# Optimization experiments

Measured on AMD Instinct MI355X. Metric: run time of the kernel, lower is better.

## Reference

```python
import jax, jax.numpy as jnp
import numpy as np
import math

R = 3  # search_radius
GROUPS = 4

def _conv(x, w):
    return jax.lax.conv_general_dilated(x, w, (1, 1), 'SAME',
                                        dimension_numbers=('NCHW', 'OIHW', 'NCHW'))

def _gn(x, g, b, eps=1e-5):
    B, C, H, W = x.shape
    xr = x.reshape(B, GROUPS, C // GROUPS, H, W)
    m = xr.mean(axis=(2, 3, 4), keepdims=True)
    v = xr.var(axis=(2, 3, 4), keepdims=True)
    xn = ((xr - m) * jax.lax.rsqrt(v + eps)).reshape(B, C, H, W)
    return xn * g.reshape(1, C, 1, 1) + b.reshape(1, C, 1, 1)

def _gelu(x):
    return jax.nn.gelu(x, approximate=False)

def _encode(x, W0, Ws, G, Bt):
    x = _gelu(_gn(_conv(x, W0), G[0], Bt[0]))
    for i in range(Ws.shape[0]):  # fixed depth-1 layers
        x = _gelu(_gn(_conv(x, Ws[i]), G[i + 1], Bt[i + 1]))
    return x

def _center_w(h, w):
    y = jnp.linspace(-1.0, 1.0, h)
    x = jnp.linspace(-1.0, 1.0, w)
    yy, xx = jnp.meshgrid(y, x, indexing='ij')
    g = jnp.exp(-(yy ** 2 + xx ** 2) / (2 * 0.5 ** 2))
    return (g / g.sum())[None, None]  # [1,1,H,W]

def _l2n(x):  # F.normalize(dim=1, eps=1e-6)
    n = jnp.sqrt(jnp.sum(x * x, axis=1, keepdims=True))
    return x / jnp.maximum(n, 1e-6)

def setup_inputs() -> dict:
    key = jax.random.key(0)
    ks = jax.random.split(key, 24)
    B, Cr, H, W, Ch, MH = 256, 6, 64, 64, 32, 128
    depth = 4
    feat_dim = Ch * 3 + 2
    s = 0.05
    return {
        'rubin_patch': jax.random.normal(ks[0], (B, Cr, H, W), jnp.float32),
        'vis_patch': jax.random.normal(ks[1], (B, 1, H, W), jnp.float32),
        'pixel_to_sky': jax.random.normal(ks[2], (B, 2, 2), jnp.float32),
        'rW0': jax.random.normal(ks[3], (Ch, Cr, 3, 3), jnp.float32) * s,
        'rWs': jax.random.normal(ks[4], (depth - 1, Ch, Ch, 3, 3), jnp.float32) * s,
        'rG': 1.0 + jax.random.normal(ks[5], (depth, Ch), jnp.float32) * s,
        'rBt': jax.random.normal(ks[6], (depth, Ch), jnp.float32) * s,
        'vW0': jax.random.normal(ks[7], (Ch, 1, 3, 3), jnp.float32) * s,
        'vWs': jax.random.normal(ks[8], (depth - 1, Ch, Ch, 3, 3), jnp.float32) * s,
        'vG': 1.0 + jax.random.normal(ks[9], (depth, Ch), jnp.float32) * s,
        'vBt': jax.random.normal(ks[10], (depth, Ch), jnp.float32) * s,
        'projR': jax.random.normal(ks[11], (Ch, Ch), jnp.float32) * s,
        'projV': jax.random.normal(ks[12], (Ch, Ch), jnp.float32) * s,
        'log_temp': jnp.array(math.log(0.05), jnp.float32),
        'W1': jax.random.normal(ks[13], (feat_dim, MH), jnp.float32) * s,
        'b1': jax.random.normal(ks[14], (MH,), jnp.float32) * s,
        'W2': jax.random.normal(ks[15], (MH, MH), jnp.float32) * s,
        'b2': jax.random.normal(ks[16], (MH,), jnp.float32) * s,
        'W3': jax.random.normal(ks[17], (MH, 3), jnp.float32) * s,
        'b3': jax.random.normal(ks[18], (3,), jnp.float32) * s,
    }

def _forward(rubin_patch, vis_patch, pixel_to_sky, rW0, rWs, rG, rBt,
             vW0, vWs, vG, vBt, projR, projV, log_temp,
             W1, b1, W2, b2, W3, b3):
    rubin_feat = _encode(rubin_patch, rW0, rWs, rG, rBt)  # [B,C,H,W]
    vis_feat = _encode(vis_patch, vW0, vWs, vG, vBt)
    B, C, H, W = rubin_feat.shape

    # --- weighted cross-correlation cost volume ---
    rubin_n = _l2n(jnp.einsum('oc,bchw->bohw', projR, rubin_feat))
    vis_n = _l2n(jnp.einsum('oc,bchw->bohw', projV, vis_feat))
    rubin_energy = jnp.sum(rubin_n * rubin_n, axis=1, keepdims=True)
    gauss = _center_w(H, W)
    sw = rubin_energy * gauss
    sw = sw / (jnp.sum(sw, axis=(2, 3), keepdims=True) + 1e-8)
    rw = rubin_n * sw  # fold weights into rubin features once
    vis_pad = jnp.pad(vis_n, ((0, 0), (0, 0), (R, R), (R, R)), mode='edge')
    scale = 1.0 / math.sqrt(float(C))
    logits = []
    for dy in range(-R, R + 1):
        for dx in range(-R, R + 1):
            sh = vis_pad[:, :, R + dy:R + dy + H, R + dx:R + dx + W]
            logits.append(jnp.sum(rw * sh, axis=(1, 2, 3)) * scale)
    logits = jnp.stack(logits, axis=1)  # [B,(2R+1)^2]

    dx_lut = jnp.array([float(dx) for dy in range(-R, R + 1) for dx in range(-R, R + 1)], jnp.float32)
    dy_lut = jnp.array([float(dy) for dy in range(-R, R + 1) for dx in range(-R, R + 1)], jnp.float32)
    temp = jnp.maximum(jnp.exp(log_temp), 1e-3)
    probs = jax.nn.softmax(logits / temp, axis=1)
    coarse_dx = jnp.sum(probs * dx_lut[None], axis=1)
    coarse_dy = jnp.sum(probs * dy_lut[None], axis=1)

    # --- center-biased pooling + MLP refine ---
    rp = jnp.sum(rubin_feat * gauss, axis=(2, 3))  # [B,C]
    vp = jnp.sum(vis_feat * gauss, axis=(2, 3))
    pooled = jnp.concatenate([rp, vp, rp - vp,
                              jnp.stack([coarse_dx, coarse_dy], axis=1)], axis=1)
    h = _gelu(pooled @ W1 + b1)
    h = _gelu(h @ W2 + b2)
    res = h @ W3 + b3  # [B,3]

    dx_px = coarse_dx + res[:, 0]
    dy_px = coarse_dy + res[:, 1]
    log_sigma = jnp.clip(res[:, 2], -6.0, 3.0)
    pix = jnp.stack([dx_px, dy_px], axis=1)
    pred_sky = jnp.einsum('bij,bj->bi', pixel_to_sky, pix)
    # pack all differentiable outputs: [dx, dy, pred_sky(2), log_sigma, logits(49)]
    return jnp.concatenate([dx_px[:, None], dy_px[:, None], pred_sky,
                            log_sigma[:, None], logits], axis=1)  # [B,54]

def reference(rubin_patch, vis_patch, pixel_to_sky, rW0, rWs, rG, rBt,
              vW0, vWs, vG, vBt, projR, projV, log_temp,
              W1, b1, W2, b2, W3, b3):
    return _forward(rubin_patch, vis_patch, pixel_to_sky, rW0, rWs, rG, rBt,
                    vW0, vWs, vG, vBt, projR, projV, log_temp,
                    W1, b1, W2, b2, W3, b3)
```

## Files before the change

### kernel.cpp

```cpp
#include <hip/hip_runtime.h>
#include <math.h>

#define HW 4096
#define NB 256

typedef __attribute__((ext_vector_type(8))) short bf16x8_t;
typedef __attribute__((ext_vector_type(16))) float f32x16_t;

__device__ __forceinline__ float gelu_f(float x) {
    float z = x * 0.70710678118654752440f;
    float az = fabsf(z);
    float t = 1.0f / fmaf(0.3275911f, az, 1.0f);
    float p = t * fmaf(t, fmaf(t, fmaf(t, fmaf(t, 1.061405429f, -1.453152027f),
                                       1.421413741f), -0.284496736f), 0.254829592f);
    float e = __expf(-az * az);
    float er = 1.0f - p * e;
    er = copysignf(er, z);
    return 0.5f * x * (1.0f + er);
}
__device__ __forceinline__ unsigned short f2bf(float f) {
    unsigned int u = __float_as_uint(f);
    unsigned int r = u + 0x7FFFu + ((u >> 16) & 1u);
    return (unsigned short)(r >> 16);
}
__device__ __forceinline__ float bf2f(unsigned short h) {
    return __uint_as_float(((unsigned int)h) << 16);
}


__global__ __launch_bounds__(256) void gauss_kernel(float* __restrict__ gauss) {
    __shared__ float sg[HW];
    __shared__ float sR[4];
    int tid = threadIdx.x;
    float part = 0.0f;
    for (int p = tid; p < HW; p += 256) {
        int y = p >> 6, x = p & 63;
        float yy = -1.0f + (2.0f / 63.0f) * (float)y;
        float xx = -1.0f + (2.0f / 63.0f) * (float)x;
        float g = expf(-(yy * yy + xx * xx) * 2.0f);
        sg[p] = g;
        part += g;
    }
#pragma unroll
    for (int off = 32; off > 0; off >>= 1) part += __shfl_down(part, off);
    if ((tid & 63) == 0) sR[tid >> 6] = part;
    __syncthreads();
    float invt = 1.0f / (sR[0] + sR[1] + sR[2] + sR[3]);
    for (int p = tid; p < HW; p += 256) gauss[p] = sg[p] * invt;
}

__global__ __launch_bounds__(256) void prep_w_kernel(
    const float* __restrict__ rWs, const float* __restrict__ vWs,
    const float* __restrict__ rW0, const float* __restrict__ vW0,
    unsigned short* __restrict__ wq) {
    int i = blockIdx.x * 256 + threadIdx.x;
    if (i >= 115712) return;
    float wv;
    if (i < 110592) {
        int j = i & 7;
        int lane = (i >> 3) & 63;
        int f = i >> 9;
        int hl = f & 1, k2 = (f >> 1) & 1, tap = (f >> 2) % 9, layer = (f >> 2) / 9;
        int co = lane & 31, hf = lane >> 5;
        int ci = k2 * 16 + hf * 8 + j;
        int ky = tap / 3, kx = tap % 3;
        wv = (layer < 3)
            ? rWs[(((size_t)layer * 32 + co) * 32 + ci) * 9 + ky * 3 + kx]
            : vWs[(((size_t)(layer - 3) * 32 + co) * 32 + ci) * 9 + ky * 3 + kx];
        unsigned short h = f2bf(wv);
        unsigned short l = f2bf(wv - bf2f(h));
        wq[i] = hl ? l : h;
        return;
    }
    int i2 = i - 110592;
    int j = i2 & 7;
    int lane = (i2 >> 3) & 63;
    int co = lane & 31, hf = lane >> 5;
    if (i2 < 4096) {
        int f = i2 >> 9;
        int hl = f & 1, ks = f >> 1;
        int q = ks * 16 + hf * 8 + j;
        wv = (q < 54) ? rW0[((size_t)co * 6 + q / 9) * 9 + q % 9] : 0.0f;
        unsigned short h = f2bf(wv);
        unsigned short l = f2bf(wv - bf2f(h));
        wq[i] = hl ? l : h;
    } else {
        int i3 = i2 - 4096;
        int f = i3 >> 9;
        int q = hf * 8 + j;
        wv = (q < 9) ? vW0[(size_t)co * 9 + q] : 0.0f;
        unsigned short h = f2bf(wv);
        unsigned short l = f2bf(wv - bf2f(h));
        wq[i] = f ? l : h;
    }
}

template <int CIN>
__global__ __launch_bounds__(128) void conv_first_m_kernel(
    const float* __restrict__ in, const unsigned short* __restrict__ wq0,
    unsigned short* __restrict__ qout, float* __restrict__ statp) {
    constexpr int KQ = CIN * 9;
    constexpr int KS = (KQ + 15) / 16;
    const int b = blockIdx.y;
    const int strip = blockIdx.x;
    const int tid = threadIdx.x;
    const int wv = tid >> 6;
    const int lane = tid & 63;
    const int m = lane & 31;
    const int hf = lane >> 5;
    const int xh32 = wv * 32;

    __shared__ __align__(16) char smem[20736];
    __shared__ float sRed[2][8];
    float* sInF = (float*)smem;

    const int y0 = strip * 4;
    const float* inb = in + (size_t)b * CIN * HW;
    for (int idx = tid; idx < CIN * 6 * 66; idx += 128) {
        int ci = idx / 396;
        int rem = idx - ci * 396;
        int r = rem / 66;
        int col = rem - r * 66;
        int gy = y0 - 1 + r;
        int gx = col - 1;
        float v = 0.0f;
        if (gy >= 0 && gy < 64 && gx >= 0 && gx < 64) v = inb[ci * HW + gy * 64 + gx];
        sInF[ci * 396 + r * 66 + col] = v;
    }

    int P[KS][8];
#pragma unroll
    for (int ks = 0; ks < KS; ++ks)
#pragma unroll
        for (int j = 0; j < 8; ++j) {
            int q = ks * 16 + hf * 8 + j;
            int ci = q / 9, tap = q - ci * 9;
            int ky = tap / 3, kx = tap - ky * 3;
            P[ks][j] = (q < KQ) ? (ci * 396 + ky * 66 + kx) : 0;
        }
    bf16x8_t Wf[KS][2];
#pragma unroll
    for (int ks = 0; ks < KS; ++ks)
#pragma unroll
        for (int hl = 0; hl < 2; ++hl)
            Wf[ks][hl] = __builtin_bit_cast(
                bf16x8_t, *(const uint4*)(wq0 + (size_t)(ks * 2 + hl) * 512 + lane * 8));
    __syncthreads();

    f32x16_t acc[4];
#pragma unroll
    for (int i = 0; i < 4; ++i)
#pragma unroll
        for (int j = 0; j < 16; ++j) acc[i][j] = 0.0f;

    const int xcol = xh32 + m;
#pragma unroll
    for (int orow = 0; orow < 4; ++orow) {
        const int obase = orow * 66 + xcol;
#pragma unroll
        for (int ks = 0; ks < KS; ++ks) {
            unsigned int pk[4];
#pragma unroll
            for (int e = 0; e < 4; ++e) {
                float v0 = sInF[P[ks][e * 2] + obase];
                float v1 = sInF[P[ks][e * 2 + 1] + obase];
                pk[e] = (unsigned)f2bf(v0) | ((unsigned)f2bf(v1) << 16);
            }
            uint4 u; u.x = pk[0]; u.y = pk[1]; u.z = pk[2]; u.w = pk[3];
            bf16x8_t A = __builtin_bit_cast(bf16x8_t, u);
            acc[orow] = __builtin_amdgcn_mfma_f32_32x32x16_bf16(A, Wf[ks][0], acc[orow], 0, 0, 0);
            acc[orow] = __builtin_amdgcn_mfma_f32_32x32x16_bf16(A, Wf[ks][1], acc[orow], 0, 0, 0);
        }
    }

    __syncthreads();
    unsigned short* lds_t = (unsigned short*)smem;
    const int co = lane & 31;
    float s1 = 0.0f, s2 = 0.0f;
#pragma unroll
    for (int orow = 0; orow < 4; ++orow) {
#pragma unroll
        for (int r = 0; r < 16; ++r) {
            int mm = (r & 3) + 8 * (r >> 2) + 4 * hf;
            int pxl = (orow << 6) + xh32 + mm;
            float v = acc[orow][r];
            s1 += v;
            s2 = fmaf(v, v, s2);
            lds_t[pxl * 40 + co] = f2bf(v);
        }
    }
    s1 += __shfl_xor(s1, 32); s2 += __shfl_xor(s2, 32);
    s1 += __shfl_xor(s1, 1);  s2 += __shfl_xor(s2, 1);
    s1 += __shfl_xor(s1, 2);  s2 += __shfl_xor(s2, 2);
    s1 += __shfl_xor(s1, 4);  s2 += __shfl_xor(s2, 4);
    if (lane < 32 && (lane & 7) == 0) {
        sRed[wv][co >> 3] = s1;
        sRed[wv][4 + (co >> 3)] = s2;
    }
    __syncthreads();
    if (tid < 8) statp[((size_t)b * 16 + strip) * 8 + tid] = sRed[0][tid] + sRed[1][tid];

    char* qb = (char*)qout + (size_t)b * 4 * HW * 16;
    const int p0 = y0 * 64;
#pragma unroll
    for (int pi = 0; pi < 2; ++pi) {
        int p = pi * 128 + tid;
#pragma unroll
        for (int s = 0; s < 4; ++s) {
            uint4 uh = *(const uint4*)(lds_t + p * 40 + s * 8);
            *(uint4*)(qb + ((size_t)(s * HW) + p0 + p) * 16) = uh;
        }
    }
}

__global__ __launch_bounds__(256) void gn_finalize_kernel(
    const float* __restrict__ statp, const float* __restrict__ gma,
    const float* __restrict__ bta, float* __restrict__ coef, int n, int ns) {
    int i = blockIdx.x * 256 + threadIdx.x;
    if (i >= n) return;
    int b = i >> 5, c = i & 31, g = c >> 3;
    float s1 = 0.0f, s2 = 0.0f;
    for (int s = 0; s < ns; ++s) {
        s1 += statp[((size_t)b * 16 + s) * 8 + g];
        s2 += statp[((size_t)b * 16 + s) * 8 + 4 + g];
    }
    const float invN = 1.0f / 32768.0f;
    float mean = s1 * invN;
    float var = s2 * invN - mean * mean;
    float rstd = rsqrtf(var + 1e-5f);
    float a = rstd * gma[c];
    float bb = bta[c] - mean * a;
    coef[i * 2 + 0] = a;
    coef[i * 2 + 1] = bb;
}

#define SLOT 80
#define ROWB (66 * SLOT)
__global__ __launch_bounds__(256) void convm_kernel(
    const unsigned short* __restrict__ qin, const float* __restrict__ coef,
    const unsigned short* __restrict__ wq,
    unsigned short* __restrict__ qout, float* __restrict__ statp) {
    const int b = blockIdx.y;
    const int strip = blockIdx.x;
    const int tid = threadIdx.x;
    const int wv = tid >> 6;
    const int lane = tid & 63;
    const int m = lane & 31;
    const int hf = lane >> 5;

    __shared__ __align__(16) char sQ[10 * ROWB];
    __shared__ float sRed[4][8];
    __shared__ float sc[64];

    const int y0 = strip * 8;
    const char* img = (const char*)qin + (size_t)b * 4 * HW * 16;

    if (tid < 64) sc[tid] = coef[b * 64 + tid];
    if (tid < 80) {
        int r = tid >> 3, side = (tid >> 2) & 1, sub = tid & 3;
        uint4 z; z.x = z.y = z.z = z.w = 0;
        *(uint4*)(sQ + r * ROWB + side * 65 * SLOT + sub * 16) = z;
    }
    __syncthreads();

    const int px = tid & 63;
    const int s_id = tid >> 6;
    const int rot = px & 3;
    float ca[8], cb[8];
#pragma unroll
    for (int e = 0; e < 8; ++e) {
        ca[e] = sc[(s_id * 8 + e) * 2 + 0];
        cb[e] = sc[(s_id * 8 + e) * 2 + 1];
    }
    uint4 ld[10];
#pragma unroll
    for (int r = 0; r < 10; ++r) {
        int gy = y0 - 1 + r;
        if (gy >= 0 && gy < 64) {
            ld[r] = *(const uint4*)(img + ((size_t)(s_id * HW) + gy * 64 + px) * 16);
        } else {
            ld[r].x = ld[r].y = ld[r].z = ld[r].w = 0;
        }
    }
    char* dstc = sQ + (px + 1) * SLOT + ((s_id + rot) & 3) * 16;
#pragma unroll
    for (int r = 0; r < 10; ++r) {
        unsigned int hd[4] = {ld[r].x, ld[r].y, ld[r].z, ld[r].w};
        unsigned int ho[4];
#pragma unroll
        for (int e = 0; e < 4; ++e) {
            float x0 = bf2f((unsigned short)(hd[e] & 0xFFFF));
            float x1 = bf2f((unsigned short)(hd[e] >> 16));
            float y0v = gelu_f(fmaf(ca[e * 2], x0, cb[e * 2]));
            float y1v = gelu_f(fmaf(ca[e * 2 + 1], x1, cb[e * 2 + 1]));
            ho[e] = (unsigned)f2bf(y0v) | ((unsigned)f2bf(y1v) << 16);
        }
        uint4 oh; oh.x = ho[0]; oh.y = ho[1]; oh.z = ho[2]; oh.w = ho[3];
        *(uint4*)(dstc + r * ROWB) = oh;
    }
    __syncthreads();

    const int rq = wv & 1;
    const int xh32 = (wv >> 1) * 32;
    f32x16_t acc[4];
#pragma unroll
    for (int i = 0; i < 4; ++i)
#pragma unroll
        for (int j = 0; j < 16; ++j) acc[i][j] = 0.0f;

    for (int kx = 0; kx < 3; ++kx) {
        bf16x8_t Wf[3][2];
#pragma unroll
        for (int ky = 0; ky < 3; ++ky)
#pragma unroll
            for (int k2 = 0; k2 < 2; ++k2) {
                int fi = (((ky * 3 + kx) * 2 + k2) * 2);
                Wf[ky][k2] = __builtin_bit_cast(
                    bf16x8_t, *(const uint4*)(wq + (size_t)fi * 512 + lane * 8));
            }
        const int slotb = xh32 + kx + m;
        const int prot = (m + kx + 3) & 3;
#pragma unroll
        for (int li = 0; li < 6; ++li) {
            const char* rowp = sQ + (rq * 4 + li) * ROWB + slotb * SLOT;
            bf16x8_t Ah[2];
#pragma unroll
            for (int k2 = 0; k2 < 2; ++k2) {
                int s = k2 * 2 + hf;
                Ah[k2] = __builtin_bit_cast(bf16x8_t, *(const uint4*)(rowp + ((s + prot) & 3) * 16));
            }
#pragma unroll
            for (int ky = 0; ky < 3; ++ky) {
                int orow = li - ky;
                if (orow < 0 || orow > 3) continue;
#pragma unroll
                for (int k2 = 0; k2 < 2; ++k2)
                    acc[orow] = __builtin_amdgcn_mfma_f32_32x32x16_bf16(Ah[k2], Wf[ky][k2], acc[orow], 0, 0, 0);
            }
        }
    }

    __syncthreads();
    unsigned short* lds_t = (unsigned short*)sQ;
    const int co = lane & 31;
    float s1 = 0.0f, s2 = 0.0f;
#pragma unroll
    for (int orow = 0; orow < 4; ++orow) {
#pragma unroll
        for (int r = 0; r < 16; ++r) {
            int mm = (r & 3) + 8 * (r >> 2) + 4 * hf;
            int pxl = (rq * 4 + orow) * 64 + xh32 + mm;
            float v = acc[orow][r];
            s1 += v;
            s2 = fmaf(v, v, s2);
            lds_t[pxl * 40 + co] = f2bf(v);
        }
    }
    s1 += __shfl_xor(s1, 32); s2 += __shfl_xor(s2, 32);
    s1 += __shfl_xor(s1, 1);  s2 += __shfl_xor(s2, 1);
    s1 += __shfl_xor(s1, 2);  s2 += __shfl_xor(s2, 2);
    s1 += __shfl_xor(s1, 4);  s2 += __shfl_xor(s2, 4);
    if (lane < 32 && (lane & 7) == 0) {
        sRed[wv][co >> 3] = s1;
        sRed[wv][4 + (co >> 3)] = s2;
    }
    __syncthreads();
    if (tid < 8)
        statp[((size_t)b * 16 + strip) * 8 + tid] =
            sRed[0][tid] + sRed[1][tid] + sRed[2][tid] + sRed[3][tid];

    char* qb = (char*)qout + (size_t)b * 4 * HW * 16;
    const int p0 = y0 * 64;
#pragma unroll
    for (int pi = 0; pi < 2; ++pi) {
        int p = pi * 256 + tid;
#pragma unroll
        for (int s = 0; s < 4; ++s) {
            uint4 uh = *(const uint4*)(lds_t + p * 40 + s * 8);
            *(uint4*)(qb + ((size_t)(s * HW) + p0 + p) * 16) = uh;
        }
    }
}

__global__ __launch_bounds__(256) void proj_kernel(
    const unsigned short* __restrict__ q, const float* __restrict__ coef,
    const float* __restrict__ pw, unsigned short* __restrict__ outn,
    float* __restrict__ poolp, float* __restrict__ E, float* __restrict__ swp,
    const float* __restrict__ gauss, int vpad) {
    int b = blockIdx.y, chunk = blockIdx.x, tid = threadIdx.x;
    int p = chunk * 256 + tid;
    __shared__ float sR[4];
    __shared__ float sc[64];
    __shared__ float red[32][257];
    if (tid < 64) sc[tid] = coef[b * 64 + tid];
    __syncthreads();
    float feat[32];
    {
        const char* qb = (const char*)q + (size_t)b * 4 * HW * 16;
#pragma unroll
        for (int s = 0; s < 4; ++s) {
            uint4 uh = *(const uint4*)(qb + ((size_t)(s * HW) + p) * 16);
            unsigned int hd[4] = {uh.x, uh.y, uh.z, uh.w};
#pragma unroll
            for (int e = 0; e < 4; ++e) {
                int c0 = s * 8 + e * 2;
                float x0 = bf2f((unsigned short)(hd[e] & 0xFFFF));
                float x1 = bf2f((unsigned short)(hd[e] >> 16));
                feat[c0] = gelu_f(fmaf(sc[c0 * 2], x0, sc[c0 * 2 + 1]));
                feat[c0 + 1] = gelu_f(fmaf(sc[(c0 + 1) * 2], x1, sc[(c0 + 1) * 2 + 1]));
            }
        }
    }
    float g = gauss[p];
#pragma unroll
    for (int c = 0; c < 32; ++c) red[c][tid] = feat[c] * g;

    float o[32];
#pragma unroll
    for (int oo = 0; oo < 32; ++oo) o[oo] = 0.0f;
    for (int c = 0; c < 32; ++c) {
        float f = feat[c];
#pragma unroll
        for (int oo = 0; oo < 32; ++oo) o[oo] = fmaf(pw[oo * 32 + c], f, o[oo]);
    }
    float nn = 0.0f;
#pragma unroll
    for (int oo = 0; oo < 32; ++oo) nn = fmaf(o[oo], o[oo], nn);
    float n = sqrtf(nn);
    float inv = 1.0f / fmaxf(n, 1e-6f);
    if (vpad) {
        int y = p >> 6, x = p & 63;
        unsigned short* vb_ = outn + (size_t)b * 32 * 4608 + y * 72 + x + 4;
#pragma unroll
        for (int oo = 0; oo < 32; ++oo) {
            unsigned short hv = f2bf(o[oo] * inv);
            unsigned short* row = vb_ + (size_t)oo * 4608;
            row[0] = hv;
            if (x == 0) { row[-4] = hv; row[-3] = hv; row[-2] = hv; row[-1] = hv; }
            if (x == 63) { row[1] = hv; row[2] = hv; row[3] = hv; row[4] = hv; }
        }
    } else {
        unsigned short* obp = outn + (size_t)b * 32 * HW + p;
#pragma unroll
        for (int oo = 0; oo < 32; ++oo) obp[(size_t)oo * HW] = f2bf(o[oo] * inv);
    }

    __syncthreads();
    if (tid < 32) {
        float s = 0.0f;
#pragma unroll 8
        for (int i = 0; i < 256; ++i) s += red[tid][i];
        poolp[((size_t)b * 16 + chunk) * 32 + tid] = s;
    }

    if (E != nullptr) {
        float e = nn * inv * inv;
        E[(size_t)b * HW + p] = e;
        float wvv = e * g;
#pragma unroll
        for (int off = 32; off > 0; off >>= 1) wvv += __shfl_down(wvv, off);
        if ((tid & 63) == 0) sR[tid >> 6] = wvv;
        __syncthreads();
        if (tid == 0) swp[b * 16 + chunk] = sR[0] + sR[1] + sR[2] + sR[3];
    }
}

__global__ __launch_bounds__(256) void logits_kernel(
    const unsigned short* __restrict__ rn, const unsigned short* __restrict__ vnp,
    const float* __restrict__ E, const float* __restrict__ swp,
    const float* __restrict__ gauss, float* __restrict__ lgpart) {
    int b = blockIdx.x, cg = blockIdx.y, tid = threadIdx.x;
    __shared__ float sR[4][49];
    float acc[49];
#pragma unroll
    for (int k = 0; k < 49; ++k) acc[k] = 0.0f;
    float ssum = 0.0f;
#pragma unroll
    for (int i = 0; i < 16; ++i) ssum += swp[b * 16 + i];
    const float scale = 0.17677669529663688f / (ssum + 1e-8f);
    const int x0 = (tid & 7) * 8;
    const float* Eb = E + (size_t)b * HW;
#pragma unroll 1
    for (int half = 0; half < 2; ++half) {
        const int y = half * 32 + (tid >> 3);
        const int pbase = y * 64 + x0;
        float4 e0 = *(const float4*)(Eb + pbase);
        float4 e1 = *(const float4*)(Eb + pbase + 4);
        float4 g0 = *(const float4*)(gauss + pbase);
        float4 g1 = *(const float4*)(gauss + pbase + 4);
        float qw[8];
        qw[0] = e0.x * g0.x * scale; qw[1] = e0.y * g0.y * scale;
        qw[2] = e0.z * g0.z * scale; qw[3] = e0.w * g0.w * scale;
        qw[4] = e1.x * g1.x * scale; qw[5] = e1.y * g1.y * scale;
        qw[6] = e1.z * g1.z * scale; qw[7] = e1.w * g1.w * scale;
#pragma unroll 1
        for (int cc = 0; cc < 4; ++cc) {
            int c = cg * 4 + cc;
            const unsigned short* rb = rn + ((size_t)b * 32 + c) * HW;
            uint4 rv = *(const uint4*)(rb + pbase);
            unsigned int rd[4] = {rv.x, rv.y, rv.z, rv.w};
            float r_[8];
            r_[0] = bf2f((unsigned short)(rd[0] & 0xFFFF)) * qw[0];
            r_[1] = bf2f((unsigned short)(rd[0] >> 16)) * qw[1];
            r_[2] = bf2f((unsigned short)(rd[1] & 0xFFFF)) * qw[2];
            r_[3] = bf2f((unsigned short)(rd[1] >> 16)) * qw[3];
            r_[4] = bf2f((unsigned short)(rd[2] & 0xFFFF)) * qw[4];
            r_[5] = bf2f((unsigned short)(rd[2] >> 16)) * qw[5];
            r_[6] = bf2f((unsigned short)(rd[3] & 0xFFFF)) * qw[6];
            r_[7] = bf2f((unsigned short)(rd[3] >> 16)) * qw[7];
            const unsigned short* vplane = vnp + ((size_t)b * 32 + c) * 4608;
#pragma unroll
            for (int dy = 0; dy < 7; ++dy) {
                int ry = y + dy - 3;
                ry = ry < 0 ? 0 : (ry > 63 ? 63 : ry);
                const unsigned short* vp = vplane + ry * 72 + x0;
                uint4 va = *(const uint4*)vp;
                uint4 vb2 = *(const uint4*)(vp + 8);
                unsigned int vd[8] = {va.x, va.y, va.z, va.w, vb2.x, vb2.y, vb2.z, vb2.w};
                float v[16];
#pragma unroll
                for (int j2 = 0; j2 < 8; ++j2) {
                    v[j2 * 2] = bf2f((unsigned short)(vd[j2] & 0xFFFF));
                    v[j2 * 2 + 1] = bf2f((unsigned short)(vd[j2] >> 16));
                }
#pragma unroll
                for (int dx = 0; dx < 7; ++dx)
#pragma unroll
                    for (int j = 0; j < 8; ++j)
                        acc[dy * 7 + dx] = fmaf(r_[j], v[j + dx + 1], acc[dy * 7 + dx]);
            }
        }
    }
#pragma unroll
    for (int k = 0; k < 49; ++k) {
#pragma unroll
        for (int off = 32; off > 0; off >>= 1) acc[k] += __shfl_down(acc[k], off);
    }
    int wid = tid >> 6;
    if ((tid & 63) == 0) {
#pragma unroll
        for (int k = 0; k < 49; ++k) sR[wid][k] = acc[k];
    }
    __syncthreads();
    if (tid < 49)
        lgpart[((size_t)b * 8 + cg) * 49 + tid] =
            sR[0][tid] + sR[1][tid] + sR[2][tid] + sR[3][tid];
}

__global__ __launch_bounds__(128) void head_kernel(
    const float* __restrict__ lg, const float* __restrict__ rpp,
    const float* __restrict__ vpp, const float* __restrict__ p2s,
    const float* __restrict__ log_temp,
    const float* __restrict__ W1, const float* __restrict__ b1,
    const float* __restrict__ W2, const float* __restrict__ b2,
    const float* __restrict__ W3, const float* __restrict__ b3,
    float* __restrict__ out) {
    int b = blockIdx.x, t = threadIdx.x;
    __shared__ float slg[49];
    __shared__ float pooled[98];
    __shared__ float h1[128], h2[128];
    __shared__ float cxy[2];
    __shared__ float res[3];
    const float* lgp = lg + (size_t)b * 8 * 49;
    if (t < 49) {
        float s = 0.0f;
#pragma unroll
        for (int g = 0; g < 8; ++g) s += lgp[g * 49 + t];
        slg[t] = s;
    }
    __syncthreads();
    if (t == 0) {
        float temp = fmaxf(expf(log_temp[0]), 0.001f);
        float invT = 1.0f / temp;
        float m = -1e30f;
        for (int k = 0; k < 49; ++k) m = fmaxf(m, slg[k] * invT);
        float s = 0.0f, pdx = 0.0f, pdy = 0.0f;
        for (int k = 0; k < 49; ++k) {
            float e = expf(slg[k] * invT - m);
            s += e;
            pdx += e * (float)((k % 7) - 3);
            pdy += e * (float)((k / 7) - 3);
        }
        cxy[0] = pdx / s;
        cxy[1] = pdy / s;
    }
    __syncthreads();
    if (t < 32) {
        float a = 0.0f, c = 0.0f;
#pragma unroll
        for (int k = 0; k < 16; ++k) {
            a += rpp[((size_t)b * 16 + k) * 32 + t];
            c += vpp[((size_t)b * 16 + k) * 32 + t];
        }
        pooled[t] = a;
        pooled[32 + t] = c;
        pooled[64 + t] = a - c;
    }
    if (t == 0) {
        pooled[96] = cxy[0];
        pooled[97] = cxy[1];
    }
    __syncthreads();
    float s1 = b1[t];
    for (int i = 0; i < 98; ++i) s1 = fmaf(pooled[i], W1[i * 128 + t], s1);
    h1[t] = gelu_f(s1);
    __syncthreads();
    float s2 = b2[t];
    for (int i = 0; i < 128; ++i) s2 = fmaf(h1[i], W2[i * 128 + t], s2);
    h2[t] = gelu_f(s2);
    __syncthreads();
    if (t < 3) {
        float r = b3[t];
        for (int i = 0; i < 128; ++i) r = fmaf(h2[i], W3[i * 3 + t], r);
        res[t] = r;
    }
    __syncthreads();
    if (t == 0) {
        float dxp = cxy[0] + res[0];
        float dyp = cxy[1] + res[1];
        float ls = fminf(fmaxf(res[2], -6.0f), 3.0f);
        const float* M = p2s + b * 4;
        float* ob = out + b * 54;
        ob[0] = dxp;
        ob[1] = dyp;
        ob[2] = M[0] * dxp + M[1] * dyp;
        ob[3] = M[2] * dxp + M[3] * dyp;
        ob[4] = ls;
    }
    if (t < 49) out[b * 54 + 5 + t] = slg[t];
}

extern "C" void kernel_launch(void* const* d_in, const int* in_sizes, int n_in,
                              void* d_out, int out_size, void* d_ws, size_t ws_size,
                              hipStream_t stream) {
    (void)in_sizes; (void)n_in; (void)out_size;
    const float* rubin = (const float*)d_in[0];
    const float* vis   = (const float*)d_in[1];
    const float* p2s   = (const float*)d_in[2];
    const float* rW0   = (const float*)d_in[3];
    const float* rWs   = (const float*)d_in[4];
    const float* rG    = (const float*)d_in[5];
    const float* rBt   = (const float*)d_in[6];
    const float* vW0   = (const float*)d_in[7];
    const float* vWs   = (const float*)d_in[8];
    const float* vG    = (const float*)d_in[9];
    const float* vBt   = (const float*)d_in[10];
    const float* projR = (const float*)d_in[11];
    const float* projV = (const float*)d_in[12];
    const float* logT  = (const float*)d_in[13];
    const float* W1    = (const float*)d_in[14];
    const float* b1    = (const float*)d_in[15];
    const float* W2    = (const float*)d_in[16];
    const float* b2    = (const float*)d_in[17];
    const float* W3    = (const float*)d_in[18];
    const float* b3    = (const float*)d_in[19];
    float* out = (float*)d_out;

    char* ws = (char*)d_ws;
    size_t off = 0;
    unsigned short* vnB = (unsigned short*)(ws + off); off += (size_t)NB * 32 * 4608 * 2;
    float* gauss  = (float*)(ws + off); off += HW * 4;
    float* statp  = (float*)(ws + off); off += (size_t)NB * 16 * 8 * 4;
    float* coefS  = (float*)(ws + off); off += (size_t)NB * 64 * 4;
    float* swp    = (float*)(ws + off); off += (size_t)NB * 16 * 4;
    float* rpp    = (float*)(ws + off); off += (size_t)NB * 16 * 32 * 4;
    float* vpp    = (float*)(ws + off); off += (size_t)NB * 16 * 32 * 4;
    float* lgbuf  = (float*)(ws + off); off += (size_t)NB * 8 * 49 * 4;
    unsigned short* wq = (unsigned short*)(ws + off); off += 115712ull * 2;
    off = (off + 255) & ~(size_t)255;
    const size_t fixed_bytes = off;
    const size_t perb = 2ull * HW * 64 + HW * 4;
    int BC = 1;
    if (ws_size > fixed_bytes + perb) {
        size_t t = (ws_size - fixed_bytes) / perb;
        BC = t > (size_t)NB ? NB : (int)t;
    }
    unsigned short* Q1 = (unsigned short*)(ws + off);
    unsigned short* Q2 = (unsigned short*)(ws + off + (size_t)BC * HW * 64);
    float* E = (float*)(ws + off + 2ull * BC * HW * 64);
    unsigned short* wq0r = wq + 110592;
    unsigned short* wq0v = wq + 114688;

    dim3 blk256(256), blk128(128);
    gauss_kernel<<<1, 256, 0, stream>>>(gauss);
    prep_w_kernel<<<452, 256, 0, stream>>>(rWs, vWs, rW0, vW0, wq);

    for (int b0 = 0; b0 < NB; b0 += BC) {
        const int bc = (NB - b0) < BC ? (NB - b0) : BC;
        dim3 cg16(16, bc), cg8(8, bc);
        const int gnblk = (bc * 32 + 255) / 256;
        float* sp = statp + (size_t)b0 * 128;
        float* cS = coefS + (size_t)b0 * 64;

        conv_first_m_kernel<1><<<cg16, blk128, 0, stream>>>(vis + (size_t)b0 * HW, wq0v, Q1, sp);
        gn_finalize_kernel<<<gnblk, 256, 0, stream>>>(sp, vG + 0, vBt + 0, cS, bc * 32, 16);
        convm_kernel<<<cg8, blk256, 0, stream>>>(Q1, cS, wq + 3 * 18432, Q2, sp);
        gn_finalize_kernel<<<gnblk, 256, 0, stream>>>(sp, vG + 32, vBt + 32, cS, bc * 32, 8);
        convm_kernel<<<cg8, blk256, 0, stream>>>(Q2, cS, wq + 4 * 18432, Q1, sp);
        gn_finalize_kernel<<<gnblk, 256, 0, stream>>>(sp, vG + 64, vBt + 64, cS, bc * 32, 8);
        convm_kernel<<<cg8, blk256, 0, stream>>>(Q1, cS, wq + 5 * 18432, Q2, sp);
        gn_finalize_kernel<<<gnblk, 256, 0, stream>>>(sp, vG + 96, vBt + 96, cS, bc * 32, 8);
        proj_kernel<<<cg16, blk256, 0, stream>>>(Q2, cS, projV, vnB + (size_t)b0 * 32 * 4608,
                                                 vpp + (size_t)b0 * 512,
                                                 (float*)nullptr, (float*)nullptr, gauss, 1);
    }

    for (int b0 = 0; b0 < NB; b0 += BC) {
        const int bc = (NB - b0) < BC ? (NB - b0) : BC;
        dim3 cg16(16, bc), cg8(8, bc);
        const int gnblk = (bc * 32 + 255) / 256;
        float* sp = statp + (size_t)b0 * 128;
        float* cS = coefS + (size_t)b0 * 64;
        float* sw = swp + (size_t)b0 * 16;
        unsigned short* rnB = Q1;

        conv_first_m_kernel<6><<<cg16, blk128, 0, stream>>>(rubin + (size_t)b0 * 6 * HW, wq0r, Q1, sp);
        gn_finalize_kernel<<<gnblk, 256, 0, stream>>>(sp, rG + 0, rBt + 0, cS, bc * 32, 16);
        convm_kernel<<<cg8, blk256, 0, stream>>>(Q1, cS, wq + 0 * 18432, Q2, sp);
        gn_finalize_kernel<<<gnblk, 256, 0, stream>>>(sp, rG + 32, rBt + 32, cS, bc * 32, 8);
        convm_kernel<<<cg8, blk256, 0, stream>>>(Q2, cS, wq + 1 * 18432, Q1, sp);
        gn_finalize_kernel<<<gnblk, 256, 0, stream>>>(sp, rG + 64, rBt + 64, cS, bc * 32, 8);
        convm_kernel<<<cg8, blk256, 0, stream>>>(Q1, cS, wq + 2 * 18432, Q2, sp);
        gn_finalize_kernel<<<gnblk, 256, 0, stream>>>(sp, rG + 96, rBt + 96, cS, bc * 32, 8);
        proj_kernel<<<cg16, blk256, 0, stream>>>(Q2, cS, projR, rnB,
                                                 rpp + (size_t)b0 * 512, E, sw, gauss, 0);
        logits_kernel<<<dim3(bc, 8), blk256, 0, stream>>>(rnB, vnB + (size_t)b0 * 32 * 4608,
                                                          E, sw, gauss,
                                                          lgbuf + (size_t)b0 * 8 * 49);
    }

    head_kernel<<<NB, 128, 0, stream>>>(lgbuf, rpp, vpp, p2s, logT, W1, b1, W2, b2, W3, b3, out);
}
```

Measured before the change: 760.0 us.

## Compute projection with split-bf16 MFMA and shuffle-based pooled reduction

The per-pixel 32x32 scalar FMA projection in proj_kernel becomes MFMA 32x32x16 bf16 instructions. Activations and weights are split into hi/lo bf16 parts to approximate fp32 accuracy, and the projection weights are pre-packed in prep_w_kernel. The gaussian-weighted channel pooling now uses wave shuffles plus a small LDS buffer instead of a 32x257 LDS transpose and a serial 256-element sum. This cuts VALU work in the projection, but adds a transpose of the MFMA outputs through LDS and a small loss of precision from the three-term split product.

Result: faster. 726.7 us (-4.4%).

```diff
diff --git a/kernel.cpp b/kernel.cpp
--- a/kernel.cpp
+++ b/kernel.cpp
@@ -52,9 +52,10 @@
 __global__ __launch_bounds__(256) void prep_w_kernel(
     const float* __restrict__ rWs, const float* __restrict__ vWs,
     const float* __restrict__ rW0, const float* __restrict__ vW0,
+    const float* __restrict__ projR, const float* __restrict__ projV,
     unsigned short* __restrict__ wq) {
     int i = blockIdx.x * 256 + threadIdx.x;
-    if (i >= 115712) return;
+    if (i >= 119808) return;
     float wv;
     if (i < 110592) {
         int j = i & 7;
@@ -72,27 +73,43 @@
         wq[i] = hl ? l : h;
         return;
     }
-    int i2 = i - 110592;
-    int j = i2 & 7;
-    int lane = (i2 >> 3) & 63;
+    if (i < 115712) {
+        int i2 = i - 110592;
+        int j = i2 & 7;
+        int lane = (i2 >> 3) & 63;
+        int co = lane & 31, hf = lane >> 5;
+        if (i2 < 4096) {
+            int f = i2 >> 9;
+            int hl = f & 1, ks = f >> 1;
+            int q = ks * 16 + hf * 8 + j;
+            wv = (q < 54) ? rW0[((size_t)co * 6 + q / 9) * 9 + q % 9] : 0.0f;
+            unsigned short h = f2bf(wv);
+            unsigned short l = f2bf(wv - bf2f(h));
+            wq[i] = hl ? l : h;
+        } else {
+            int i3 = i2 - 4096;
+            int f = i3 >> 9;
+            int q = hf * 8 + j;
+            wv = (q < 9) ? vW0[(size_t)co * 9 + q] : 0.0f;
+            unsigned short h = f2bf(wv);
+            unsigned short l = f2bf(wv - bf2f(h));
+            wq[i] = f ? l : h;
+        }
+        return;
+    }
+    int i4 = i - 115712;
+    const float* pw = (i4 < 2048) ? projR : projV;
+    int r = i4 & 2047;
+    int j = r & 7;
+    int lane = (r >> 3) & 63;
+    int f = r >> 9;
+    int hl = f & 1, k2 = f >> 1;
     int co = lane & 31, hf = lane >> 5;
-    if (i2 < 4096) {
-        int f = i2 >> 9;
-        int hl = f & 1, ks = f >> 1;
-        int q = ks * 16 + hf * 8 + j;
-        wv = (q < 54) ? rW0[((size_t)co * 6 + q / 9) * 9 + q % 9] : 0.0f;
-        unsigned short h = f2bf(wv);
-        unsigned short l = f2bf(wv - bf2f(h));
-        wq[i] = hl ? l : h;
-    } else {
-        int i3 = i2 - 4096;
-        int f = i3 >> 9;
-        int q = hf * 8 + j;
-        wv = (q < 9) ? vW0[(size_t)co * 9 + q] : 0.0f;
-        unsigned short h = f2bf(wv);
-        unsigned short l = f2bf(wv - bf2f(h));
-        wq[i] = f ? l : h;
-    }
+    int ci = k2 * 16 + hf * 8 + j;
+    wv = pw[(size_t)co * 32 + ci];
+    unsigned short h = f2bf(wv);
+    unsigned short l = f2bf(wv - bf2f(h));
+    wq[i] = hl ? l : h;
 }
 
 template <int CIN>
@@ -384,48 +401,115 @@
 
 __global__ __launch_bounds__(256) void proj_kernel(
     const unsigned short* __restrict__ q, const float* __restrict__ coef,
-    const float* __restrict__ pw, unsigned short* __restrict__ outn,
+    const unsigned short* __restrict__ wqp, unsigned short* __restrict__ outn,
     float* __restrict__ poolp, float* __restrict__ E, float* __restrict__ swp,
     const float* __restrict__ gauss, int vpad) {
     int b = blockIdx.y, chunk = blockIdx.x, tid = threadIdx.x;
-    int p = chunk * 256 + tid;
+    const int wv = tid >> 6, lane = tid & 63;
+    const int ln = lane & 31, hf = lane >> 5;
+    __shared__ float sc[64];
+    __shared__ float lds_o[256 * 33];
+    __shared__ float poolw[4][32];
     __shared__ float sR[4];
-    __shared__ float sc[64];
-    __shared__ float red[32][257];
     if (tid < 64) sc[tid] = coef[b * 64 + tid];
     __syncthreads();
-    float feat[32];
-    {
-        const char* qb = (const char*)q + (size_t)b * 4 * HW * 16;
-#pragma unroll
-        for (int s = 0; s < 4; ++s) {
-            uint4 uh = *(const uint4*)(qb + ((size_t)(s * HW) + p) * 16);
+
+    const char* qb = (const char*)q + (size_t)b * 4 * HW * 16;
+    const int pb0 = chunk * 256 + wv * 64;
+
+    bf16x8_t Bf[2][2];
+#pragma unroll
+    for (int k2 = 0; k2 < 2; ++k2)
+#pragma unroll
+        for (int hl = 0; hl < 2; ++hl)
+            Bf[k2][hl] = __builtin_bit_cast(
+                bf16x8_t, *(const uint4*)(wqp + (size_t)(k2 * 2 + hl) * 512 + lane * 8));
+
+    float psum[2][8];
+#pragma unroll
+    for (int k2 = 0; k2 < 2; ++k2)
+#pragma unroll
+        for (int j = 0; j < 8; ++j) psum[k2][j] = 0.0f;
+
+    f32x16_t acc[2];
+#pragma unroll
+    for (int i = 0; i < 2; ++i)
+#pragma unroll
+        for (int j = 0; j < 16; ++j) acc[i][j] = 0.0f;
+
+#pragma unroll
+    for (int t = 0; t < 2; ++t) {
+        int px = pb0 + t * 32 + ln;
+        float g = gauss[px];
+#pragma unroll
+        for (int k2 = 0; k2 < 2; ++k2) {
+            int s = k2 * 2 + hf;
+            uint4 uh = *(const uint4*)(qb + ((size_t)(s * HW) + px) * 16);
             unsigned int hd[4] = {uh.x, uh.y, uh.z, uh.w};
+            unsigned int ah[4], al[4];
 #pragma unroll
             for (int e = 0; e < 4; ++e) {
                 int c0 = s * 8 + e * 2;
                 float x0 = bf2f((unsigned short)(hd[e] & 0xFFFF));
                 float x1 = bf2f((unsigned short)(hd[e] >> 16));
-                feat[c0] = gelu_f(fmaf(sc[c0 * 2], x0, sc[c0 * 2 + 1]));
-                feat[c0 + 1] = gelu_f(fmaf(sc[(c0 + 1) * 2], x1, sc[(c0 + 1) * 2 + 1]));
+                float f0 = gelu_f(fmaf(sc[c0 * 2], x0, sc[c0 * 2 + 1]));
+                float f1 = gelu_f(fmaf(sc[c0 * 2 + 2], x1, sc[c0 * 2 + 3]));
+                psum[k2][e * 2] = fmaf(f0, g, psum[k2][e * 2]);
+                psum[k2][e * 2 + 1] = fmaf(f1, g, psum[k2][e * 2 + 1]);
+                unsigned short h0 = f2bf(f0), h1 = f2bf(f1);
+                unsigned short l0 = f2bf(f0 - bf2f(h0)), l1 = f2bf(f1 - bf2f(h1));
+                ah[e] = (unsigned)h0 | ((unsigned)h1 << 16);
+                al[e] = (unsigned)l0 | ((unsigned)l1 << 16);
             }
-        }
-    }
-    float g = gauss[p];
-#pragma unroll
-    for (int c = 0; c < 32; ++c) red[c][tid] = feat[c] * g;
-
+            uint4 uah; uah.x = ah[0]; uah.y = ah[1]; uah.z = ah[2]; uah.w = ah[3];
+            uint4 ual; ual.x = al[0]; ual.y = al[1]; ual.z = al[2]; ual.w = al[3];
+            bf16x8_t Ah = __builtin_bit_cast(bf16x8_t, uah);
+            bf16x8_t Al = __builtin_bit_cast(bf16x8_t, ual);
+            acc[t] = __builtin_amdgcn_mfma_f32_32x32x16_bf16(Ah, Bf[k2][0], acc[t], 0, 0, 0);
+            acc[t] = __builtin_amdgcn_mfma_f32_32x32x16_bf16(Ah, Bf[k2][1], acc[t], 0, 0, 0);
+            acc[t] = __builtin_amdgcn_mfma_f32_32x32x16_bf16(Al, Bf[k2][0], acc[t], 0, 0, 0);
+        }
+    }
+
+#pragma unroll
+    for (int t = 0; t < 2; ++t)
+#pragma unroll
+        for (int r = 0; r < 16; ++r) {
+            int mm = (r & 3) + 8 * (r >> 2) + 4 * hf;
+            lds_o[(wv * 64 + t * 32 + mm) * 33 + ln] = acc[t][r];
+        }
+
+#pragma unroll
+    for (int k2 = 0; k2 < 2; ++k2)
+#pragma unroll
+        for (int j = 0; j < 8; ++j) {
+            float v = psum[k2][j];
+            v += __shfl_xor(v, 1); v += __shfl_xor(v, 2);
+            v += __shfl_xor(v, 4); v += __shfl_xor(v, 8);
+            v += __shfl_xor(v, 16);
+            psum[k2][j] = v;
+        }
+    if (ln == 0) {
+#pragma unroll
+        for (int k2 = 0; k2 < 2; ++k2)
+#pragma unroll
+            for (int j = 0; j < 8; ++j)
+                poolw[wv][k2 * 16 + hf * 8 + j] = psum[k2][j];
+    }
+    __syncthreads();
+    if (tid < 32) {
+        float s = poolw[0][tid] + poolw[1][tid] + poolw[2][tid] + poolw[3][tid];
+        poolp[((size_t)b * 16 + chunk) * 32 + tid] = s;
+    }
+
+    int p = chunk * 256 + tid;
     float o[32];
-#pragma unroll
-    for (int oo = 0; oo < 32; ++oo) o[oo] = 0.0f;
-    for (int c = 0; c < 32; ++c) {
-        float f = feat[c];
-#pragma unroll
-        for (int oo = 0; oo < 32; ++oo) o[oo] = fmaf(pw[oo * 32 + c], f, o[oo]);
-    }
     float nn = 0.0f;
 #pragma unroll
-    for (int oo = 0; oo < 32; ++oo) nn = fmaf(o[oo], o[oo], nn);
+    for (int oo = 0; oo < 32; ++oo) {
+        o[oo] = lds_o[tid * 33 + oo];
+        nn = fmaf(o[oo], o[oo], nn);
+    }
     float n = sqrtf(nn);
     float inv = 1.0f / fmaxf(n, 1e-6f);
     if (vpad) {
@@ -445,18 +529,10 @@
         for (int oo = 0; oo < 32; ++oo) obp[(size_t)oo * HW] = f2bf(o[oo] * inv);
     }
 
-    __syncthreads();
-    if (tid < 32) {
-        float s = 0.0f;
-#pragma unroll 8
-        for (int i = 0; i < 256; ++i) s += red[tid][i];
-        poolp[((size_t)b * 16 + chunk) * 32 + tid] = s;
-    }
-
     if (E != nullptr) {
         float e = nn * inv * inv;
         E[(size_t)b * HW + p] = e;
-        float wvv = e * g;
+        float wvv = e * gauss[p];
 #pragma unroll
         for (int off = 32; off > 0; off >>= 1) wvv += __shfl_down(wvv, off);
         if ((tid & 63) == 0) sR[tid >> 6] = wvv;
@@ -666,7 +742,7 @@
     float* rpp    = (float*)(ws + off); off += (size_t)NB * 16 * 32 * 4;
     float* vpp    = (float*)(ws + off); off += (size_t)NB * 16 * 32 * 4;
     float* lgbuf  = (float*)(ws + off); off += (size_t)NB * 8 * 49 * 4;
-    unsigned short* wq = (unsigned short*)(ws + off); off += 115712ull * 2;
+    unsigned short* wq = (unsigned short*)(ws + off); off += 119808ull * 2;
     off = (off + 255) & ~(size_t)255;
     const size_t fixed_bytes = off;
     const size_t perb = 2ull * HW * 64 + HW * 4;
@@ -680,10 +756,12 @@
     float* E = (float*)(ws + off + 2ull * BC * HW * 64);
     unsigned short* wq0r = wq + 110592;
     unsigned short* wq0v = wq + 114688;
+    unsigned short* wqpR = wq + 115712;
+    unsigned short* wqpV = wq + 117760;
 
     dim3 blk256(256), blk128(128);
     gauss_kernel<<<1, 256, 0, stream>>>(gauss);
-    prep_w_kernel<<<452, 256, 0, stream>>>(rWs, vWs, rW0, vW0, wq);
+    prep_w_kernel<<<468, 256, 0, stream>>>(rWs, vWs, rW0, vW0, projR, projV, wq);
 
     for (int b0 = 0; b0 < NB; b0 += BC) {
         const int bc = (NB - b0) < BC ? (NB - b0) : BC;
@@ -700,7 +778,7 @@
         gn_finalize_kernel<<<gnblk, 256, 0, stream>>>(sp, vG + 64, vBt + 64, cS, bc * 32, 8);
         convm_kernel<<<cg8, blk256, 0, stream>>>(Q1, cS, wq + 5 * 18432, Q2, sp);
         gn_finalize_kernel<<<gnblk, 256, 0, stream>>>(sp, vG + 96, vBt + 96, cS, bc * 32, 8);
-        proj_kernel<<<cg16, blk256, 0, stream>>>(Q2, cS, projV, vnB + (size_t)b0 * 32 * 4608,
+        proj_kernel<<<cg16, blk256, 0, stream>>>(Q2, cS, wqpV, vnB + (size_t)b0 * 32 * 4608,
                                                  vpp + (size_t)b0 * 512,
                                                  (float*)nullptr, (float*)nullptr, gauss, 1);
     }
@@ -722,7 +800,7 @@
         gn_finalize_kernel<<<gnblk, 256, 0, stream>>>(sp, rG + 64, rBt + 64, cS, bc * 32, 8);
         convm_kernel<<<cg8, blk256, 0, stream>>>(Q1, cS, wq + 2 * 18432, Q2, sp);
         gn_finalize_kernel<<<gnblk, 256, 0, stream>>>(sp, rG + 96, rBt + 96, cS, bc * 32, 8);
-        proj_kernel<<<cg16, blk256, 0, stream>>>(Q2, cS, projR, rnB,
+        proj_kernel<<<cg16, blk256, 0, stream>>>(Q2, cS, wqpR, rnB,
                                                  rpp + (size_t)b0 * 512, E, sw, gauss, 0);
         logits_kernel<<<dim3(bc, 8), blk256, 0, stream>>>(rnB, vnB + (size_t)b0 * 32 * 4608,
                                                           E, sw, gauss,
```
